# Kernel optimization log

Hardware: AMD Instinct MI355X
Metric: run time of the kernel (lower is better)

The kernel has to match this reference:

```python
import jax, jax.numpy as jnp
import numpy as np

B, S, H, N = 2, 2048, 1024, 16
HN = H // N  # head dim = 64
EPS = 1e-12


def setup_inputs() -> dict:
    key = jax.random.key(0)
    ks = jax.random.split(key, 8)
    scale = 0.02
    return {
        "hidden_states": jax.random.normal(ks[0], (B, S, H), dtype=jnp.float32),
        "attention_mask": jnp.zeros((B, 1, 1, S), dtype=jnp.float32),
        "W_qkv": jax.random.normal(ks[1], (3 * H, H), dtype=jnp.float32) * scale,
        "b_qkv": jnp.zeros((3 * H,), dtype=jnp.float32),
        "W_out": jax.random.normal(ks[2], (H, H), dtype=jnp.float32) * scale,
        "b_out": jnp.zeros((H,), dtype=jnp.float32),
        "ln_gamma": jnp.ones((H,), dtype=jnp.float32),
        "ln_beta": jnp.zeros((H,), dtype=jnp.float32),
    }


def reference(hidden_states, attention_mask, W_qkv, b_qkv, W_out, b_out, ln_gamma, ln_beta):
    # QKV projection: torch Linear => x @ W.T + b
    qkv = jnp.einsum("bsh,oh->bso", hidden_states, W_qkv) + b_qkv  # [B,S,3H]
    q, k, v = jnp.split(qkv, 3, axis=-1)

    def heads(t):  # [B,S,H] -> [B,N,S,HN]
        return t.reshape(B, S, N, HN).transpose(0, 2, 1, 3)

    q, k, v = heads(q), heads(k), heads(v)
    nf = jnp.sqrt(jnp.sqrt(jnp.float32(HN)))
    scores = jnp.einsum("bnsd,bntd->bnst", q / nf, k / nf) + attention_mask  # [B,N,S,S]
    probs = jax.nn.softmax(scores, axis=-1)
    ctx = jnp.einsum("bnst,bntd->bnsd", probs, v)  # [B,N,S,HN]
    ctx = ctx.transpose(0, 2, 1, 3).reshape(B, S, H)

    # output dense + residual + LayerNorm
    out = jnp.einsum("bsh,oh->bso", ctx, W_out) + b_out
    x = out + hidden_states
    mean = jnp.mean(x, axis=-1, keepdims=True)
    var = jnp.mean(jnp.square(x - mean), axis=-1, keepdims=True)
    return (x - mean) * jax.lax.rsqrt(var + EPS) * ln_gamma + ln_beta
```

## Files before the change

### kernel.cpp

```cpp
#include <hip/hip_runtime.h>
#include <hip/hip_bf16.h>
#include <math.h>

#define Bq  2
#define Sq  2048
#define Hq  1024
#define Nq  16
#define HNq 64
#define Mq  (Bq*Sq)
#define H3q (3*Hq)

#define LOG2E 1.44269504088896340736f

typedef __attribute__((ext_vector_type(8))) short           short8;
typedef __attribute__((ext_vector_type(4))) short           short4s;
typedef __attribute__((ext_vector_type(8))) unsigned short  ushortx8;
typedef __attribute__((ext_vector_type(4))) unsigned short  ushortx4;
typedef __attribute__((ext_vector_type(4))) float           floatx4;

__device__ __forceinline__ unsigned short f2bf(float f) {
    union { float f; unsigned int u; } x; x.f = f;
    unsigned int r = (x.u + 0x7fffu + ((x.u >> 16) & 1u)) >> 16;
    return (unsigned short)r;
}

__device__ __forceinline__ unsigned int pkbf(float a, float b) {
    float2 t; t.x = a; t.y = b;
    __hip_bfloat162 h = __float22bfloat162_rn(t);
    union { __hip_bfloat162 h; unsigned int u; } c; c.h = h;
    return c.u;
}

__device__ __forceinline__ float bf2f(unsigned short v) {
    union { unsigned int u; float f; } x; x.u = (unsigned int)v << 16;
    return x.f;
}

__device__ __forceinline__ float fexp2(float x) {
    float r;
    asm("v_exp_f32 %0, %1" : "=v"(r) : "v"(x));
    return r;
}

__device__ __forceinline__ void gload16(const unsigned short* g, unsigned short* l) {
    __builtin_amdgcn_global_load_lds(
        (__attribute__((address_space(1))) void*)(unsigned long long)(g),
        (__attribute__((address_space(3))) void*)(unsigned int)(unsigned long long)(l),
        16, 0, 0);
}

__device__ __forceinline__ int swz(int r) { return (r ^ (r >> 2)) & 3; }

#define N_HID ((size_t)Mq * Hq)
#define N_HW  (N_HID + (size_t)H3q * Hq)
#define N_ALL (N_HW + (size_t)Hq * Hq)
#define CVT_BLKS ((int)(N_ALL / 2048))

__global__ __launch_bounds__(256) void cvt_all(
    const float* __restrict__ hidden, const float* __restrict__ wqkv,
    const float* __restrict__ wout, const float* __restrict__ mask,
    unsigned short* __restrict__ dst, unsigned short* __restrict__ em2)
{
    const int bid = blockIdx.x;
    if (bid >= CVT_BLKS) {
        const int t0   = ((bid - CVT_BLKS) * 256 + threadIdx.x) * 8;
        const int b    = t0 >> 11;
        const int t2   = t0 & 2047;
        const int kt   = t2 >> 6;
        const int t3   = t2 & 63;
        const int ks   = t3 >> 5;
        const int quad = (t3 >> 3) & 3;
        const int kb   = kt * 64 + ks * 32 + quad * 4;
        const float* mp = mask + (size_t)b * Sq + kb;
        float4 m0 = *(const float4*)(mp);
        float4 m1 = *(const float4*)(mp + 16);
        union { unsigned int u[4]; ushortx8 s; } o;
        o.u[0] = pkbf(fexp2(m0.x * LOG2E), fexp2(m0.y * LOG2E));
        o.u[1] = pkbf(fexp2(m0.z * LOG2E), fexp2(m0.w * LOG2E));
        o.u[2] = pkbf(fexp2(m1.x * LOG2E), fexp2(m1.y * LOG2E));
        o.u[3] = pkbf(fexp2(m1.z * LOG2E), fexp2(m1.w * LOG2E));
        *(ushortx8*)(em2 + t0) = o.s;
        return;
    }
    size_t i = ((size_t)bid * 256 + threadIdx.x) * 8;
    const float* src;
    if (i < N_HID)      src = hidden + i;
    else if (i < N_HW)  src = wqkv + (i - N_HID);
    else                src = wout + (i - N_HW);
    float4 a = *(const float4*)(src);
    float4 b = *(const float4*)(src + 4);
    union { unsigned int u[4]; ushortx8 s; } o;
    o.u[0] = pkbf(a.x, a.y); o.u[1] = pkbf(a.z, a.w);
    o.u[2] = pkbf(b.x, b.y); o.u[3] = pkbf(b.z, b.w);
    *(ushortx8*)(dst + i) = o.s;
}

#define TM 128
#define TN 128
#define TK 32

__global__ __launch_bounds__(256) void gemm_mfma_qkv(
    const unsigned short* __restrict__ A, const unsigned short* __restrict__ Bw,
    const float* __restrict__ bias, const float* __restrict__ mask,
    unsigned short* __restrict__ Qb, unsigned short* __restrict__ Kd,
    unsigned short* __restrict__ V5, int K)
{
    __shared__ unsigned short As[3][TM][TK];
    __shared__ unsigned short Bs[3][TN][TK];

    const int tid = threadIdx.x;
    const int w = tid >> 6, lane = tid & 63;
    const int l15 = lane & 15, quad = lane >> 4;
    const int wr = (w & 1) * 64;
    const int wc = (w >> 1) * 64;
    const int row0 = blockIdx.y * TM;
    const int col0 = blockIdx.x * TN;

    const int srow16 = lane >> 2;
    const int sgd    = lane & 3;
    const int sgsrc  = (sgd ^ swz(srow16)) * 8;

    floatx4 acc[4][4];
    #pragma unroll
    for (int i = 0; i < 4; i++)
        #pragma unroll
        for (int j = 0; j < 4; j++) acc[i][j] = (floatx4){0.f,0.f,0.f,0.f};

    const int aswz = swz(l15) * 8;
    const int NK = K / TK;

    #pragma unroll
    for (int t = 0; t < 2; t++) {
        #pragma unroll
        for (int c = 0; c < 2; c++) {
            int seg = w * 2 + c;
            int r = seg * 16 + srow16;
            gload16(A  + (size_t)(row0 + r) * K + t * TK + sgsrc, &As[t][seg * 16][0]);
            gload16(Bw + (size_t)(col0 + r) * K + t * TK + sgsrc, &Bs[t][seg * 16][0]);
        }
    }

    #pragma unroll 1
    for (int k = 0; k < NK; ++k) {
        if (k + 1 < NK) asm volatile("s_waitcnt vmcnt(4)" ::: "memory");
        else            asm volatile("s_waitcnt vmcnt(0)" ::: "memory");
        __builtin_amdgcn_s_barrier();
        __builtin_amdgcn_sched_barrier(0);

        const int cur = k % 3;
        if (k + 2 < NK) {
            const int nb  = (k + 2) % 3;
            const int k0n = (k + 2) * TK;
            #pragma unroll
            for (int c = 0; c < 2; c++) {
                int seg = w * 2 + c;
                int r = seg * 16 + srow16;
                gload16(A  + (size_t)(row0 + r) * K + k0n + sgsrc, &As[nb][seg * 16][0]);
                gload16(Bw + (size_t)(col0 + r) * K + k0n + sgsrc, &Bs[nb][seg * 16][0]);
            }
        }
        __builtin_amdgcn_sched_barrier(0);

        short8 af[4], bf[4];
        #pragma unroll
        for (int i = 0; i < 4; i++)
            af[i] = *(const short8*)&As[cur][wr + i * 16 + l15][(quad * 8) ^ aswz];
        #pragma unroll
        for (int j = 0; j < 4; j++)
            bf[j] = *(const short8*)&Bs[cur][wc + j * 16 + l15][(quad * 8) ^ aswz];
        __builtin_amdgcn_s_setprio(1);
        #pragma unroll
        for (int i = 0; i < 4; i++)
            #pragma unroll
            for (int j = 0; j < 4; j++)
                acc[i][j] = __builtin_amdgcn_mfma_f32_16x16x32_bf16(af[i], bf[j], acc[i][j], 0, 0, 0);
        __builtin_amdgcn_s_setprio(0);
    }

    const int cls = col0 >> 10;

    if (cls == 2) {
        #pragma unroll
        for (int i = 0; i < 4; i++) {
            const int rb = row0 + wr + i * 16 + quad * 4;
            const int b  = rb >> 11;
            const int s  = rb & (Sq - 1);
            const int kt32 = s >> 6;
            const int sw   = s & 63;
            const int kg   = sw >> 2;
            const int ks   = kg >> 3;
            const int q2   = kg & 3;
            const int hi   = (kg >> 2) & 1;
            float expm[4];
            #pragma unroll
            for (int rr = 0; rr < 4; rr++)
                expm[rr] = fexp2(mask[(size_t)b * Sq + s + rr] * LOG2E);
            #pragma unroll
            for (int j = 0; j < 4; j++) {
                const int c  = col0 + wc + j * 16 + l15;
                const int c2 = c - 2 * Hq;
                const int n  = c2 >> 6, d = c2 & 63;
                const int dt = d >> 4, dl = d & 15;
                const float bia = bias[c];
                ushortx4 o;
                #pragma unroll
                for (int rr = 0; rr < 4; rr++)
                    o[rr] = f2bf((acc[i][j][rr] + bia) * expm[rr]);
                const size_t off = (((size_t)(b * Nq + n) * 32 + kt32) << 12)
                                 + (size_t)((ks * 16 + dt * 4 + q2) * 128 + dl * 8 + hi * 4);
                *(ushortx4*)&V5[off] = o;
            }
        }
    } else {
        unsigned short* __restrict__ dst = (cls == 0) ? Qb : Kd;
        const int cshift = (cls == 0) ? 0 : Hq;
        const float qs = (cls == 0) ? (0.125f * LOG2E) : 1.0f;
        #pragma unroll
        for (int i = 0; i < 4; i++) {
            const int rb = row0 + wr + i * 16 + quad * 4;
            #pragma unroll
            for (int j = 0; j < 4; j++) {
                const int c = col0 + wc + j * 16 + l15;
                const float bia = bias[c];
                #pragma unroll
                for (int rr = 0; rr < 4; rr++)
                    dst[(size_t)(rb + rr) * Hq + (c - cshift)] =
                        f2bf((acc[i][j][rr] + bia) * qs);
            }
        }
    }
}

__global__ __launch_bounds__(256) void gemm_mfma_out(
    const unsigned short* __restrict__ A, const unsigned short* __restrict__ Bw,
    const float* __restrict__ bias, const float* __restrict__ res,
    unsigned short* __restrict__ X, int M, int Nd, int K)
{
    __shared__ unsigned short As[3][TM][TK];
    __shared__ unsigned short Bs[3][TN][TK];

    const int tid = threadIdx.x;
    const int w = tid >> 6, lane = tid & 63;
    const int l15 = lane & 15, quad = lane >> 4;
    const int wr = (w & 1) * 64;
    const int wc = (w >> 1) * 64;
    const int row0 = blockIdx.y * TM;
    const int col0 = blockIdx.x * TN;

    const int srow16 = lane >> 2;
    const int sgd    = lane & 3;
    const int sgsrc  = (sgd ^ swz(srow16)) * 8;

    floatx4 acc[4][4];
    #pragma unroll
    for (int i = 0; i < 4; i++)
        #pragma unroll
        for (int j = 0; j < 4; j++) acc[i][j] = (floatx4){0.f,0.f,0.f,0.f};

    const int aswz = swz(l15) * 8;
    const int NK = K / TK;

    #pragma unroll
    for (int t = 0; t < 2; t++) {
        #pragma unroll
        for (int c = 0; c < 2; c++) {
            int seg = w * 2 + c;
            int r = seg * 16 + srow16;
            gload16(A  + (size_t)(row0 + r) * K + t * TK + sgsrc, &As[t][seg * 16][0]);
            gload16(Bw + (size_t)(col0 + r) * K + t * TK + sgsrc, &Bs[t][seg * 16][0]);
        }
    }

    #pragma unroll 1
    for (int k = 0; k < NK; ++k) {
        if (k + 1 < NK) asm volatile("s_waitcnt vmcnt(4)" ::: "memory");
        else            asm volatile("s_waitcnt vmcnt(0)" ::: "memory");
        __builtin_amdgcn_s_barrier();
        __builtin_amdgcn_sched_barrier(0);

        const int cur = k % 3;
        if (k + 2 < NK) {
            const int nb  = (k + 2) % 3;
            const int k0n = (k + 2) * TK;
            #pragma unroll
            for (int c = 0; c < 2; c++) {
                int seg = w * 2 + c;
                int r = seg * 16 + srow16;
                gload16(A  + (size_t)(row0 + r) * K + k0n + sgsrc, &As[nb][seg * 16][0]);
                gload16(Bw + (size_t)(col0 + r) * K + k0n + sgsrc, &Bs[nb][seg * 16][0]);
            }
        }
        __builtin_amdgcn_sched_barrier(0);

        short8 af[4], bf[4];
        #pragma unroll
        for (int i = 0; i < 4; i++)
            af[i] = *(const short8*)&As[cur][wr + i * 16 + l15][(quad * 8) ^ aswz];
        #pragma unroll
        for (int j = 0; j < 4; j++)
            bf[j] = *(const short8*)&Bs[cur][wc + j * 16 + l15][(quad * 8) ^ aswz];
        __builtin_amdgcn_s_setprio(1);
        #pragma unroll
        for (int i = 0; i < 4; i++)
            #pragma unroll
            for (int j = 0; j < 4; j++)
                acc[i][j] = __builtin_amdgcn_mfma_f32_16x16x32_bf16(af[i], bf[j], acc[i][j], 0, 0, 0);
        __builtin_amdgcn_s_setprio(0);
    }

    #pragma unroll
    for (int i = 0; i < 4; i++) {
        const int rb = row0 + wr + i * 16 + quad * 4;
        #pragma unroll
        for (int j = 0; j < 4; j++) {
            const int c = col0 + wc + j * 16 + l15;
            const float bia = bias[c];
            #pragma unroll
            for (int rr = 0; rr < 4; rr++) {
                X[(size_t)(rb + rr) * Nd + c] =
                    f2bf(acc[i][j][rr] + bia + res[(size_t)(rb + rr) * Nd + c]);
            }
        }
    }
}

#define KTILES 16

__device__ __forceinline__ floatx4 mfma16(short8 a, short8 b, floatx4 c) {
    return __builtin_amdgcn_mfma_f32_16x16x32_bf16(a, b, c, 0, 0, 0);
}

__device__ __forceinline__ void do_lpv(
    const short8 (&pf0)[2], const short8 (&pf1)[2], const short8 (&mf)[2],
    const unsigned short* Vt,
    floatx4 (&oacc0)[4], floatx4 (&oacc1)[4],
    floatx4 &lacc0, floatx4 &lacc1)
{
    __builtin_amdgcn_s_setprio(1);
    lacc0 = mfma16(mf[0], pf0[0], lacc0);
    lacc0 = mfma16(mf[1], pf0[1], lacc0);
    lacc1 = mfma16(mf[0], pf1[0], lacc1);
    lacc1 = mfma16(mf[1], pf1[1], lacc1);
    #pragma unroll
    for (int dt = 0; dt < 4; dt++) {
        short8 vlo = *(const short8*)(Vt + dt * 512);
        short8 vhi = *(const short8*)(Vt + 2048 + dt * 512);
        oacc0[dt] = mfma16(vlo, pf0[0], oacc0[dt]);
        oacc1[dt] = mfma16(vlo, pf1[0], oacc1[dt]);
        oacc0[dt] = mfma16(vhi, pf0[1], oacc0[dt]);
        oacc1[dt] = mfma16(vhi, pf1[1], oacc1[dt]);
    }
    __builtin_amdgcn_s_setprio(0);
}

template<bool HAVER, bool PREF>
__device__ __forceinline__ void attn_body(
    int kt,
    unsigned short (&KsL)[2][64][64],
    unsigned short (&VsL)[3][4096],
    const unsigned short* kp, size_t kstep,
    const unsigned short* Vb, const unsigned short* e2b,
    int w, int l15, int quad, int lane,
    const short8 (&qf0)[2], const short8 (&qf1)[2],
    const short8 (&pfR0)[2], const short8 (&pfR1)[2], const short8 (&mfR)[2],
    short8 (&pfW0)[2], short8 (&pfW1)[2], short8 (&mfW)[2],
    floatx4 (&oacc0)[4], floatx4 (&oacc1)[4],
    floatx4 &lacc0, floatx4 &lacc1)
{
    asm volatile("s_waitcnt vmcnt(0)" ::: "memory");
    __builtin_amdgcn_s_barrier();
    __builtin_amdgcn_sched_barrier(0);

    if (PREF) {
        const unsigned short* kpn = kp + (size_t)(kt + 1) * kstep;
        gload16(kpn,                  &KsL[(kt + 1) & 1][w * 16][0]);
        gload16(kpn + (size_t)8 * Hq, &KsL[(kt + 1) & 1][w * 16 + 8][0]);
        const unsigned short* vpn = Vb + (size_t)(kt + 1) * 4096 + w * 1024 + lane * 8;
        unsigned short* vd = &VsL[(kt + 1) % 3][w * 1024];
        gload16(vpn,       vd);
        gload16(vpn + 512, vd + 512);
    }
    __builtin_amdgcn_sched_barrier(0);

    const unsigned short* ep = e2b + kt * 64;
    mfW[0] = *(const short8*)(ep + quad * 8);
    mfW[1] = *(const short8*)(ep + 32 + quad * 8);

    floatx4 s0[4], s1[4];
    #pragma unroll
    for (int ct = 0; ct < 4; ct++) {
        s0[ct] = (floatx4){0.f,0.f,0.f,0.f};
        s1[ct] = (floatx4){0.f,0.f,0.f,0.f};
    }
    __builtin_amdgcn_s_setprio(1);
    #pragma unroll
    for (int ks = 0; ks < 2; ks++) {
        #pragma unroll
        for (int ct = 0; ct < 4; ct++) {
            short8 af = *(const short8*)&KsL[kt & 1][ct * 16 + l15][((4 * ks + quad) ^ (l15 & 7)) * 8];
            s0[ct] = mfma16(af, qf0[ks], s0[ct]);
            s1[ct] = mfma16(af, qf1[ks], s1[ct]);
        }
    }
    __builtin_amdgcn_s_setprio(0);

    #pragma unroll
    for (int ks = 0; ks < 2; ks++) {
        union { unsigned int u[4]; short8 s; } pk;
        #pragma unroll
        for (int h = 0; h < 2; h++) {
            const int ct = ks * 2 + h;
            pk.u[h * 2]     = pkbf(fexp2(s0[ct][0]), fexp2(s0[ct][1]));
            pk.u[h * 2 + 1] = pkbf(fexp2(s0[ct][2]), fexp2(s0[ct][3]));
        }
        pfW0[ks] = pk.s;
    }
    #pragma unroll
    for (int ks = 0; ks < 2; ks++) {
        union { unsigned int u[4]; short8 s; } pk;
        #pragma unroll
        for (int h = 0; h < 2; h++) {
            const int ct = ks * 2 + h;
            pk.u[h * 2]     = pkbf(fexp2(s1[ct][0]), fexp2(s1[ct][1]));
            pk.u[h * 2 + 1] = pkbf(fexp2(s1[ct][2]), fexp2(s1[ct][3]));
        }
        pfW1[ks] = pk.s;
    }

    if (HAVER)
        do_lpv(pfR0, pfR1, mfR, &VsL[(kt - 1) % 3][0] + lane * 8,
               oacc0, oacc1, lacc0, lacc1);
}

__global__ __launch_bounds__(256) void attn_mfma(
    const unsigned short* __restrict__ Qb, const unsigned short* __restrict__ Kd,
    const unsigned short* __restrict__ V5, const unsigned short* __restrict__ em2,
    unsigned short* __restrict__ Opart, float* __restrict__ Lpart)
{
    __shared__ unsigned short Ks[2][64][64];
    __shared__ unsigned short Vs[3][4096];

    const int tid  = threadIdx.x;
    const int w    = tid >> 6;
    const int lane = tid & 63;
    const int l15  = lane & 15;
    const int quad = lane >> 4;

    const int i_    = blockIdx.x;
    const int gl8   = i_ & 7;
    const int rest  = i_ >> 3;
    const int qtile = rest & 15;
    const int g     = (rest >> 4) * 8 + gl8;
    const int bn    = g >> 1;
    const int z     = g & 1;
    const int n     = bn & 15;
    const int b     = bn >> 4;

    const int kbase = z * (KTILES * 64);

    short8 qf0[2], qf1[2];
    {
        const int qrow0 = qtile * 128 + w * 16 + l15;
        const unsigned short* qp = Qb + (size_t)(b * Sq + qrow0) * Hq + n * HNq + quad * 8;
        qf0[0] = *(const short8*)(qp);
        qf0[1] = *(const short8*)(qp + 32);
        qp += (size_t)64 * Hq;
        qf1[0] = *(const short8*)(qp);
        qf1[1] = *(const short8*)(qp + 32);
    }

    floatx4 oacc0[4], oacc1[4];
    #pragma unroll
    for (int dt = 0; dt < 4; dt++) {
        oacc0[dt] = (floatx4){0.f,0.f,0.f,0.f};
        oacc1[dt] = (floatx4){0.f,0.f,0.f,0.f};
    }
    floatx4 lacc0 = (floatx4){0.f,0.f,0.f,0.f};
    floatx4 lacc1 = (floatx4){0.f,0.f,0.f,0.f};

    const int krow8 = lane >> 3;
    const int kgr   = (lane & 7) ^ (krow8 & 7);
    const unsigned short* kp = Kd + (size_t)(b * Sq + kbase + w * 16 + krow8) * Hq
                                  + n * HNq + kgr * 8;
    const size_t kstep = (size_t)64 * Hq;

    const unsigned short* Vb  = V5 + ((size_t)(b * Nq + n) * 32 + z * KTILES) * 4096;
    const unsigned short* e2b = em2 + (size_t)(b * 32 + z * KTILES) * 64;

    gload16(kp,                  &Ks[0][w * 16][0]);
    gload16(kp + (size_t)8 * Hq, &Ks[0][w * 16 + 8][0]);
    {
        const unsigned short* vp0 = Vb + w * 1024 + lane * 8;
        gload16(vp0,       &Vs[0][w * 1024]);
        gload16(vp0 + 512, &Vs[0][w * 1024] + 512);
    }

    short8 pfA0[2], pfA1[2], mfA[2];
    short8 pfB0[2], pfB1[2], mfB[2];

    attn_body<false, true>(0, Ks, Vs, kp, kstep, Vb, e2b, w, l15, quad, lane,
        qf0, qf1, pfB0, pfB1, mfB, pfA0, pfA1, mfA, oacc0, oacc1, lacc0, lacc1);

    #pragma unroll 1
    for (int kt = 1; kt < KTILES - 1; kt += 2) {
        attn_body<true, true>(kt, Ks, Vs, kp, kstep, Vb, e2b, w, l15, quad, lane,
            qf0, qf1, pfA0, pfA1, mfA, pfB0, pfB1, mfB, oacc0, oacc1, lacc0, lacc1);
        attn_body<true, true>(kt + 1, Ks, Vs, kp, kstep, Vb, e2b, w, l15, quad, lane,
            qf0, qf1, pfB0, pfB1, mfB, pfA0, pfA1, mfA, oacc0, oacc1, lacc0, lacc1);
    }
    attn_body<true, false>(KTILES - 1, Ks, Vs, kp, kstep, Vb, e2b, w, l15, quad, lane,
        qf0, qf1, pfA0, pfA1, mfA, pfB0, pfB1, mfB, oacc0, oacc1, lacc0, lacc1);
    do_lpv(pfB0, pfB1, mfB, &Vs[(KTILES - 1) % 3][0] + lane * 8,
           oacc0, oacc1, lacc0, lacc1);

    unsigned short* Ow = Opart + (size_t)z * Mq * Hq;
    #pragma unroll
    for (int sub = 0; sub < 2; sub++) {
        const float l_i = sub ? lacc1[0] : lacc0[0];
        const int qrow = qtile * 128 + sub * 64 + w * 16 + l15;
        if (quad == 0)
            Lpart[(size_t)z * Mq * Nq + (size_t)(b * Sq + qrow) * Nq + n] = l_i;
        #pragma unroll
        for (int dt = 0; dt < 4; dt++) {
            const floatx4 oa = sub ? oacc1[dt] : oacc0[dt];
            union { unsigned int u[2]; ushortx4 s; } o;
            o.u[0] = pkbf(oa[0], oa[1]);
            o.u[1] = pkbf(oa[2], oa[3]);
            const int col = n * HNq + dt * 16 + quad * 4;
            *(ushortx4*)&Ow[(size_t)(b * Sq + qrow) * Hq + col] = o.s;
        }
    }
}

__global__ __launch_bounds__(256) void attn_merge(
    const unsigned short* __restrict__ Opart, const float* __restrict__ Lpart,
    unsigned short* __restrict__ ctx)
{
    const size_t idx = ((size_t)blockIdx.x * 256 + threadIdx.x) * 4;
    const int row = (int)(idx >> 10);
    const int n   = ((int)idx >> 6) & 15;
    const float l = Lpart[(size_t)row * Nq + n]
                  + Lpart[(size_t)Mq * Nq + (size_t)row * Nq + n];
    const float inv = 1.0f / l;
    ushortx4 a = *(const ushortx4*)(Opart + idx);
    ushortx4 c = *(const ushortx4*)(Opart + (size_t)Mq * Hq + idx);
    union { unsigned int u[2]; ushortx4 s; } o;
    o.u[0] = pkbf((bf2f(a[0]) + bf2f(c[0])) * inv, (bf2f(a[1]) + bf2f(c[1])) * inv);
    o.u[1] = pkbf((bf2f(a[2]) + bf2f(c[2])) * inv, (bf2f(a[3]) + bf2f(c[3])) * inv);
    *(ushortx4*)(ctx + idx) = o.s;
}

__global__ __launch_bounds__(256) void ln_kernel(
    const unsigned short* __restrict__ X, const float* __restrict__ gamma,
    const float* __restrict__ beta, float* __restrict__ out)
{
    const int row = blockIdx.x;
    const int c0  = threadIdx.x * 4;
    ushortx4 xv = *(const ushortx4*)(X + (size_t)row * Hq + c0);
    float vals[4];
    float lsum = 0.0f;
    #pragma unroll
    for (int i = 0; i < 4; i++) { vals[i] = bf2f(xv[i]); lsum += vals[i]; }

    __shared__ float red[8];
    const int wid = threadIdx.x >> 6, lane = threadIdx.x & 63;

    float s = lsum;
    #pragma unroll
    for (int off = 32; off >= 1; off >>= 1) s += __shfl_xor(s, off, 64);
    if (lane == 0) red[wid] = s;
    __syncthreads();
    const float mean = (red[0] + red[1] + red[2] + red[3]) * (1.0f / Hq);

    float v = 0.0f;
    #pragma unroll
    for (int i = 0; i < 4; i++) { float d = vals[i] - mean; v += d * d; }
    #pragma unroll
    for (int off = 32; off >= 1; off >>= 1) v += __shfl_xor(v, off, 64);
    if (lane == 0) red[4 + wid] = v;
    __syncthreads();
    const float var  = (red[4] + red[5] + red[6] + red[7]) * (1.0f / Hq);
    const float rstd = rsqrtf(var + 1e-12f);

    float4 gm = *(const float4*)(gamma + c0);
    float4 bt = *(const float4*)(beta + c0);
    float4 o;
    o.x = (vals[0] - mean) * rstd * gm.x + bt.x;
    o.y = (vals[1] - mean) * rstd * gm.y + bt.y;
    o.z = (vals[2] - mean) * rstd * gm.z + bt.z;
    o.w = (vals[3] - mean) * rstd * gm.w + bt.w;
    *(float4*)(out + (size_t)row * Hq + c0) = o;
}

extern "C" void kernel_launch(void* const* d_in, const int* in_sizes, int n_in,
                              void* d_out, int out_size, void* d_ws, size_t ws_size,
                              hipStream_t stream)
{
    const float* hidden = (const float*)d_in[0];
    const float* mask   = (const float*)d_in[1];
    const float* W_qkv  = (const float*)d_in[2];
    const float* b_qkv  = (const float*)d_in[3];
    const float* W_out  = (const float*)d_in[4];
    const float* b_out  = (const float*)d_in[5];
    const float* gamma  = (const float*)d_in[6];
    const float* beta   = (const float*)d_in[7];
    float* out = (float*)d_out;

    const size_t nHid  = (size_t)Mq * Hq;
    const size_t nWq   = (size_t)H3q * Hq;
    const size_t nWo   = (size_t)Hq * Hq;
    const size_t nCtx  = (size_t)Mq * Hq;

    unsigned short* hidden_bf = (unsigned short*)d_ws;
    unsigned short* Wqkv_bf   = hidden_bf + nHid;
    unsigned short* Wout_bf   = Wqkv_bf + nWq;
    unsigned short* qb        = Wout_bf + nWo;
    unsigned short* kd        = qb + nHid;
    unsigned short* v5        = kd + nHid;
    unsigned short* ctx_bf    = v5 + nHid;
    unsigned short* x_bf      = ctx_bf + nCtx;
    unsigned short* opart     = x_bf + nHid;
    float*          lpart     = (float*)(opart + 2 * nHid);
    unsigned short* em2       = (unsigned short*)(lpart + 2 * (size_t)Mq * Nq);

    dim3 blk(256);

    cvt_all<<<dim3(CVT_BLKS + 2), blk, 0, stream>>>(
        hidden, W_qkv, W_out, mask, hidden_bf, em2);

    gemm_mfma_qkv<<<dim3(H3q / TN, Mq / TM), blk, 0, stream>>>(
        hidden_bf, Wqkv_bf, b_qkv, mask, qb, kd, v5, Hq);

    attn_mfma<<<dim3(1024), blk, 0, stream>>>(
        qb, kd, v5, em2, opart, lpart);

    attn_merge<<<dim3((int)(nCtx / 1024)), blk, 0, stream>>>(
        opart, lpart, ctx_bf);

    gemm_mfma_out<<<dim3(Hq / TN, Mq / TM), blk, 0, stream>>>(
        ctx_bf, Wout_bf, b_out, hidden, x_bf, Mq, Hq, Hq);

    ln_kernel<<<dim3(Mq), blk, 0, stream>>>(x_bf, gamma, beta, out);
}
```

Measured before the change: 203.3 us.

## Pre-tile K per head in QKV epilogue and enlarge QKV GEMM tile to 256 rows

The QKV GEMM now uses 512-thread blocks with a 256x128 tile, so each B tile is reused across more rows. Its K epilogue writes K into a per-head, per-64-row-tile, XOR-swizzled contiguous layout (K5), the same way V was already stored. The attention kernel then streams each K tile as contiguous 8KB chunks instead of strided rows of the full hidden-width matrix. The trade-offs are scalar scattered 2-byte stores in the K epilogue, a larger LDS footprint, and fewer GEMM blocks, which could lower occupancy.

```diff
diff --git a/kernel.cpp b/kernel.cpp
--- a/kernel.cpp
+++ b/kernel.cpp
@@ -98,22 +98,23 @@
 #define TM 128
 #define TN 128
 #define TK 32
-
-__global__ __launch_bounds__(256) void gemm_mfma_qkv(
+#define G1M 256
+
+__global__ __launch_bounds__(512) void gemm_mfma_qkv(
     const unsigned short* __restrict__ A, const unsigned short* __restrict__ Bw,
     const float* __restrict__ bias, const float* __restrict__ mask,
-    unsigned short* __restrict__ Qb, unsigned short* __restrict__ Kd,
+    unsigned short* __restrict__ Qb, unsigned short* __restrict__ K5,
     unsigned short* __restrict__ V5, int K)
 {
-    __shared__ unsigned short As[3][TM][TK];
+    __shared__ unsigned short As[3][G1M][TK];
     __shared__ unsigned short Bs[3][TN][TK];
 
     const int tid = threadIdx.x;
     const int w = tid >> 6, lane = tid & 63;
     const int l15 = lane & 15, quad = lane >> 4;
-    const int wr = (w & 1) * 64;
-    const int wc = (w >> 1) * 64;
-    const int row0 = blockIdx.y * TM;
+    const int wr = (w & 3) * 64;
+    const int wc = (w >> 2) * 64;
+    const int row0 = blockIdx.y * G1M;
     const int col0 = blockIdx.x * TN;
 
     const int srow16 = lane >> 2;
@@ -135,14 +136,15 @@
         for (int c = 0; c < 2; c++) {
             int seg = w * 2 + c;
             int r = seg * 16 + srow16;
-            gload16(A  + (size_t)(row0 + r) * K + t * TK + sgsrc, &As[t][seg * 16][0]);
-            gload16(Bw + (size_t)(col0 + r) * K + t * TK + sgsrc, &Bs[t][seg * 16][0]);
-        }
+            gload16(A + (size_t)(row0 + r) * K + t * TK + sgsrc, &As[t][seg * 16][0]);
+        }
+        int rB = w * 16 + srow16;
+        gload16(Bw + (size_t)(col0 + rB) * K + t * TK + sgsrc, &Bs[t][w * 16][0]);
     }
 
     #pragma unroll 1
     for (int k = 0; k < NK; ++k) {
-        if (k + 1 < NK) asm volatile("s_waitcnt vmcnt(4)" ::: "memory");
+        if (k + 1 < NK) asm volatile("s_waitcnt vmcnt(3)" ::: "memory");
         else            asm volatile("s_waitcnt vmcnt(0)" ::: "memory");
         __builtin_amdgcn_s_barrier();
         __builtin_amdgcn_sched_barrier(0);
@@ -155,9 +157,10 @@
             for (int c = 0; c < 2; c++) {
                 int seg = w * 2 + c;
                 int r = seg * 16 + srow16;
-                gload16(A  + (size_t)(row0 + r) * K + k0n + sgsrc, &As[nb][seg * 16][0]);
-                gload16(Bw + (size_t)(col0 + r) * K + k0n + sgsrc, &Bs[nb][seg * 16][0]);
+                gload16(A + (size_t)(row0 + r) * K + k0n + sgsrc, &As[nb][seg * 16][0]);
             }
+            int rB = w * 16 + srow16;
+            gload16(Bw + (size_t)(col0 + rB) * K + k0n + sgsrc, &Bs[nb][w * 16][0]);
         }
         __builtin_amdgcn_sched_barrier(0);
 
@@ -211,10 +214,31 @@
                 *(ushortx4*)&V5[off] = o;
             }
         }
+    } else if (cls == 1) {
+        #pragma unroll
+        for (int i = 0; i < 4; i++) {
+            const int rb = row0 + wr + i * 16 + quad * 4;
+            #pragma unroll
+            for (int j = 0; j < 4; j++) {
+                const int c  = col0 + wc + j * 16 + l15;
+                const int c2 = c - Hq;
+                const int n  = c2 >> 6, d = c2 & 63;
+                const float bia = bias[c];
+                #pragma unroll
+                for (int rr = 0; rr < 4; rr++) {
+                    const int srow = rb + rr;
+                    const int b    = srow >> 11;
+                    const int s    = srow & (Sq - 1);
+                    const int kt32 = s >> 6;
+                    const int r    = s & 63;
+                    const size_t off = (((size_t)(b * Nq + n) * 32 + kt32) << 12)
+                                     + (size_t)(r * 64 + (((d >> 3) ^ (r & 7)) * 8 + (d & 7)));
+                    K5[off] = f2bf(acc[i][j][rr] + bia);
+                }
+            }
+        }
     } else {
-        unsigned short* __restrict__ dst = (cls == 0) ? Qb : Kd;
-        const int cshift = (cls == 0) ? 0 : Hq;
-        const float qs = (cls == 0) ? (0.125f * LOG2E) : 1.0f;
+        const float qs = 0.125f * LOG2E;
         #pragma unroll
         for (int i = 0; i < 4; i++) {
             const int rb = row0 + wr + i * 16 + quad * 4;
@@ -224,7 +248,7 @@
                 const float bia = bias[c];
                 #pragma unroll
                 for (int rr = 0; rr < 4; rr++)
-                    dst[(size_t)(rb + rr) * Hq + (c - cshift)] =
+                    Qb[(size_t)(rb + rr) * Hq + c] =
                         f2bf((acc[i][j][rr] + bia) * qs);
             }
         }
@@ -358,8 +382,7 @@
     int kt,
     unsigned short (&KsL)[2][64][64],
     unsigned short (&VsL)[3][4096],
-    const unsigned short* kp, size_t kstep,
-    const unsigned short* Vb, const unsigned short* e2b,
+    const unsigned short* Kb, const unsigned short* Vb, const unsigned short* e2b,
     int w, int l15, int quad, int lane,
     const short8 (&qf0)[2], const short8 (&qf1)[2],
     const short8 (&pfR0)[2], const short8 (&pfR1)[2], const short8 (&mfR)[2],
@@ -372,9 +395,9 @@
     __builtin_amdgcn_sched_barrier(0);
 
     if (PREF) {
-        const unsigned short* kpn = kp + (size_t)(kt + 1) * kstep;
-        gload16(kpn,                  &KsL[(kt + 1) & 1][w * 16][0]);
-        gload16(kpn + (size_t)8 * Hq, &KsL[(kt + 1) & 1][w * 16 + 8][0]);
+        const unsigned short* kpn = Kb + (size_t)(kt + 1) * 4096 + w * 1024 + lane * 8;
+        gload16(kpn,       &KsL[(kt + 1) & 1][w * 16][0]);
+        gload16(kpn + 512, &KsL[(kt + 1) & 1][w * 16 + 8][0]);
         const unsigned short* vpn = Vb + (size_t)(kt + 1) * 4096 + w * 1024 + lane * 8;
         unsigned short* vd = &VsL[(kt + 1) % 3][w * 1024];
         gload16(vpn,       vd);
@@ -433,7 +456,7 @@
 }
 
 __global__ __launch_bounds__(256) void attn_mfma(
-    const unsigned short* __restrict__ Qb, const unsigned short* __restrict__ Kd,
+    const unsigned short* __restrict__ Qb, const unsigned short* __restrict__ K5,
     const unsigned short* __restrict__ V5, const unsigned short* __restrict__ em2,
     unsigned short* __restrict__ Opart, float* __restrict__ Lpart)
 {
@@ -456,8 +479,6 @@
     const int n     = bn & 15;
     const int b     = bn >> 4;
 
-    const int kbase = z * (KTILES * 64);
-
     short8 qf0[2], qf1[2];
     {
         const int qrow0 = qtile * 128 + w * 16 + l15;
@@ -478,18 +499,14 @@
     floatx4 lacc0 = (floatx4){0.f,0.f,0.f,0.f};
     floatx4 lacc1 = (floatx4){0.f,0.f,0.f,0.f};
 
-    const int krow8 = lane >> 3;
-    const int kgr   = (lane & 7) ^ (krow8 & 7);
-    const unsigned short* kp = Kd + (size_t)(b * Sq + kbase + w * 16 + krow8) * Hq
-                                  + n * HNq + kgr * 8;
-    const size_t kstep = (size_t)64 * Hq;
-
+    const unsigned short* Kb  = K5 + ((size_t)(b * Nq + n) * 32 + z * KTILES) * 4096;
     const unsigned short* Vb  = V5 + ((size_t)(b * Nq + n) * 32 + z * KTILES) * 4096;
     const unsigned short* e2b = em2 + (size_t)(b * 32 + z * KTILES) * 64;
 
-    gload16(kp,                  &Ks[0][w * 16][0]);
-    gload16(kp + (size_t)8 * Hq, &Ks[0][w * 16 + 8][0]);
     {
+        const unsigned short* kp0 = Kb + w * 1024 + lane * 8;
+        gload16(kp0,       &Ks[0][w * 16][0]);
+        gload16(kp0 + 512, &Ks[0][w * 16 + 8][0]);
         const unsigned short* vp0 = Vb + w * 1024 + lane * 8;
         gload16(vp0,       &Vs[0][w * 1024]);
         gload16(vp0 + 512, &Vs[0][w * 1024] + 512);
@@ -498,17 +515,17 @@
     short8 pfA0[2], pfA1[2], mfA[2];
     short8 pfB0[2], pfB1[2], mfB[2];
 
-    attn_body<false, true>(0, Ks, Vs, kp, kstep, Vb, e2b, w, l15, quad, lane,
+    attn_body<false, true>(0, Ks, Vs, Kb, Vb, e2b, w, l15, quad, lane,
         qf0, qf1, pfB0, pfB1, mfB, pfA0, pfA1, mfA, oacc0, oacc1, lacc0, lacc1);
 
     #pragma unroll 1
     for (int kt = 1; kt < KTILES - 1; kt += 2) {
-        attn_body<true, true>(kt, Ks, Vs, kp, kstep, Vb, e2b, w, l15, quad, lane,
+        attn_body<true, true>(kt, Ks, Vs, Kb, Vb, e2b, w, l15, quad, lane,
             qf0, qf1, pfA0, pfA1, mfA, pfB0, pfB1, mfB, oacc0, oacc1, lacc0, lacc1);
-        attn_body<true, true>(kt + 1, Ks, Vs, kp, kstep, Vb, e2b, w, l15, quad, lane,
+        attn_body<true, true>(kt + 1, Ks, Vs, Kb, Vb, e2b, w, l15, quad, lane,
             qf0, qf1, pfB0, pfB1, mfB, pfA0, pfA1, mfA, oacc0, oacc1, lacc0, lacc1);
     }
-    attn_body<true, false>(KTILES - 1, Ks, Vs, kp, kstep, Vb, e2b, w, l15, quad, lane,
+    attn_body<true, false>(KTILES - 1, Ks, Vs, Kb, Vb, e2b, w, l15, quad, lane,
         qf0, qf1, pfA0, pfA1, mfA, pfB0, pfB1, mfB, oacc0, oacc1, lacc0, lacc1);
     do_lpv(pfB0, pfB1, mfB, &Vs[(KTILES - 1) % 3][0] + lane * 8,
            oacc0, oacc1, lacc0, lacc1);
@@ -615,8 +632,8 @@
     unsigned short* Wqkv_bf   = hidden_bf + nHid;
     unsigned short* Wout_bf   = Wqkv_bf + nWq;
     unsigned short* qb        = Wout_bf + nWo;
-    unsigned short* kd        = qb + nHid;
-    unsigned short* v5        = kd + nHid;
+    unsigned short* k5        = qb + nHid;
+    unsigned short* v5        = k5 + nHid;
     unsigned short* ctx_bf    = v5 + nHid;
     unsigned short* x_bf      = ctx_bf + nCtx;
     unsigned short* opart     = x_bf + nHid;
@@ -628,11 +645,11 @@
     cvt_all<<<dim3(CVT_BLKS + 2), blk, 0, stream>>>(
         hidden, W_qkv, W_out, mask, hidden_bf, em2);
 
-    gemm_mfma_qkv<<<dim3(H3q / TN, Mq / TM), blk, 0, stream>>>(
-        hidden_bf, Wqkv_bf, b_qkv, mask, qb, kd, v5, Hq);
+    gemm_mfma_qkv<<<dim3(H3q / TN, Mq / G1M), dim3(512), 0, stream>>>(
+        hidden_bf, Wqkv_bf, b_qkv, mask, qb, k5, v5, Hq);
 
     attn_mfma<<<dim3(1024), blk, 0, stream>>>(
-        qb, kd, v5, em2, opart, lpart);
+        qb, k5, v5, em2, opart, lpart);
 
     attn_merge<<<dim3((int)(nCtx / 1024)), blk, 0, stream>>>(
         opart, lpart, ctx_bf);
```

After: 202.8 us. Within noise of the previous version (-0.3%).
